# Optimization experiments

Hardware: AMD Instinct MI355X
Metric: run time of the kernel (lower is better)

The kernel has to match this reference:

```python
import jax, jax.numpy as jnp
import numpy as np

N = 200000      # active voxels
CIN = 96        # in_channels == out_channels (identity residual path)
CMID = 192      # max(in,out) * channel_multiplier
OFF = 27        # kernel_size**3 offsets
EPS = 1e-5      # BatchNorm eps


def setup_inputs() -> dict:
    key = jax.random.key(0)
    ks = jax.random.split(key, 6)
    x = jax.random.normal(ks[0], (N, CIN), jnp.float32)
    idx = jax.random.randint(ks[1], (OFF, N), 0, N, jnp.int32)
    mask = jax.random.randint(ks[2], (OFF, N), 0, 2, jnp.int32)
    W1 = jax.random.normal(ks[3], (OFF, CIN, CMID), jnp.float32) / np.float32(np.sqrt(OFF * CIN))
    W2 = jax.random.normal(ks[4], (OFF, CMID, CIN), jnp.float32) / np.float32(np.sqrt(OFF * CMID))
    g1 = jnp.ones((CMID,), jnp.float32)
    b1 = jnp.zeros((CMID,), jnp.float32)
    g2 = jnp.ones((CIN,), jnp.float32)
    b2 = jnp.zeros((CIN,), jnp.float32)
    return {"x": x, "idx": idx, "mask": mask, "W1": W1, "g1": g1, "b1": b1,
            "W2": W2, "g2": g2, "b2": b2}


def _sparse_conv(x, idx, mask, W):
    """Explicit-GEMM sparse conv: per-offset gather -> GEMM -> accumulate.
    x: [N, Cin], idx/mask: [OFF, N], W: [OFF, Cin, Cout] -> [N, Cout]."""
    n = x.shape[0]
    cout = W.shape[-1]

    def body(acc, off):
        i, m, w = off
        g = jnp.where(m[:, None] > 0, x[i], jnp.zeros((), x.dtype))  # gather [N, Cin]
        return acc + g @ w, None

    out, _ = jax.lax.scan(body, jnp.zeros((n, cout), x.dtype), (idx, mask, W))
    return out


def _bn(x, gamma, beta):
    # BatchNorm1d in training mode: batch statistics over the voxel dim.
    mu = jnp.mean(x, axis=0)
    var = jnp.var(x, axis=0)
    return gamma * (x - mu) * jax.lax.rsqrt(var + EPS) + beta


def reference(x, idx, mask, W1, g1, b1, W2, g2, b2):
    h = jax.nn.relu(_bn(_sparse_conv(x, idx, mask, W1), g1, b1))
    h = _bn(_sparse_conv(h, idx, mask, W2), g2, b2)
    return jax.nn.relu(h + x)  # identity residual (in_channels == out_channels)
```

## Files before the change

kernel.cpp:

```cpp
#include <hip/hip_runtime.h>
#include <hip/hip_bf16.h>

typedef unsigned short u16;
typedef __attribute__((ext_vector_type(8))) short short8;
typedef __attribute__((ext_vector_type(4))) float f32x4;
typedef __attribute__((ext_vector_type(8))) unsigned short ushort8v;

#define NVOX 200000
#define NOFF 27
#define NBLK 1563

__device__ __forceinline__ u16 f2bf(float f) {
    __hip_bfloat16 h = __float2bfloat16(f);
    return *reinterpret_cast<u16*>(&h);
}
__device__ __forceinline__ float bf2f(u16 u) {
    union { unsigned int i; float f; } v;
    v.i = ((unsigned int)u) << 16;
    return v.f;
}

#define GLOAD_LDS16(g, l)                                                     \
    __builtin_amdgcn_global_load_lds(                                         \
        (const __attribute__((address_space(1))) unsigned int*)(g),           \
        (__attribute__((address_space(3))) unsigned int*)(l), 16, 0, 0)

__global__ __launch_bounds__(256) void prep_kernel(
    const float* __restrict__ x, const float* __restrict__ W1,
    const float* __restrict__ W2, u16* __restrict__ xb,
    u16* __restrict__ w1t, u16* __restrict__ w2t, float* __restrict__ zbuf)
{
    const int XV = NVOX * 96 / 4;
    const int WC = 62208;
    int t = blockIdx.x * 256 + threadIdx.x;
    if (blockIdx.x == 0 && threadIdx.x < 64) zbuf[threadIdx.x] = 0.f;
    if (t < XV) {
        float4 v = *(const float4*)(x + (size_t)t * 4);
        ushort4 o;
        o.x = f2bf(v.x); o.y = f2bf(v.y); o.z = f2bf(v.z); o.w = f2bf(v.w);
        *(ushort4*)(xb + (size_t)t * 4) = o;
    } else if (t < XV + WC) {
        int j = t - XV;
        int lane = j & 63, rest = j >> 6;
        int nco = rest % 12, rest2 = rest / 12;
        int ks = rest2 % 3, off = rest2 / 3;
        int co = nco * 16 + (lane & 15);
        int kb = ks * 32 + (lane >> 4) * 8;
        const float* src = W1 + (size_t)off * 18432 + (size_t)kb * 192 + co;
        ushort8v ov;
#pragma unroll
        for (int jj = 0; jj < 8; ++jj) ov[jj] = f2bf(src[(size_t)jj * 192]);
        *(ushort8v*)(w1t + (size_t)j * 8) = ov;
    } else if (t < XV + 2 * WC) {
        int j = t - XV - WC;
        int lane = j & 63, rest = j >> 6;
        int nco = rest % 6, rest2 = rest / 6;
        int kk = rest2 % 6, off = rest2 / 6;
        int co = nco * 16 + (lane & 15);
        int kb = kk * 32 + (lane >> 4) * 8;
        const float* src = W2 + (size_t)off * 18432 + (size_t)kb * 96 + co;
        ushort8v ov;
#pragma unroll
        for (int jj = 0; jj < 8; ++jj) ov[jj] = f2bf(src[(size_t)jj * 96]);
        *(ushort8v*)(w2t + (size_t)j * 8) = ov;
    }
}

template<int COUT, int WN, int HFDIV>
__global__ __launch_bounds__(512, 4) void conv_mfma(
    const u16* __restrict__ xb, const int* __restrict__ idxp,
    const int* __restrict__ mskp, const u16* __restrict__ Wt,
    const float* __restrict__ zbuf, u16* __restrict__ hout,
    float* __restrict__ part)
{
    constexpr int CIN  = 96 * HFDIV;
    constexpr int WM   = 8 / WN;
    constexpr int FM   = 128 / (WM * 16);
    constexpr int FN   = COUT / (WN * 16);
    constexpr int NCO  = COUT / 16;
    constexpr int SG   = NOFF * HFDIV;
    constexpr int BUFU = 128 * 96;

    __shared__ u16 ldsA[2 * BUFU];
    __shared__ int lsrcL[NOFF * 128];

    const int tid  = threadIdx.x;
    const int row0 = blockIdx.x * 128;
    const int lane = tid & 63;
    const int wid  = tid >> 6;
    const int wm   = wid / WN;
    const int wn   = wid % WN;
    const int lr   = lane & 15;
    const int lk   = lane >> 4;

#pragma unroll
    for (int it = 0; it < 7; ++it) {
        int l = it * 512 + tid;
        if (l < NOFF * 128) {
            int o = l >> 7, r = row0 + (l & 127);
            int rr = r < NVOX ? r : NVOX - 1;
            int mv = mskp[(size_t)o * NVOX + rr];
            int iv = idxp[(size_t)o * NVOX + rr];
            lsrcL[l] = (r < NVOX && mv > 0) ? iv : -1;
        }
    }

    int aRow[3], aGcOff[3];
#pragma unroll
    for (int it = 0; it < 3; ++it) {
        int l = it * 512 + tid;
        int r = l / 12, c = l % 12;
        aRow[it] = r;
        aGcOff[it] = ((c + r) % 12) * 8;
    }
    int aBase[FM], d0m[FM];
#pragma unroll
    for (int m = 0; m < FM; ++m) {
        int r = wm * (FM * 16) + m * 16 + lr;
        aBase[m] = r * 96;
        d0m[m] = lk - (r % 12);
    }
    const u16* wtw = Wt + (size_t)(wn * FN) * 512 + (size_t)lane * 8;
    const int ldsWaveBase = (tid & ~63) * 8;

    f32x4 acc[FM][FN];
#pragma unroll
    for (int m = 0; m < FM; ++m)
#pragma unroll
        for (int n = 0; n < FN; ++n)
            acc[m][n] = (f32x4){0.f, 0.f, 0.f, 0.f};

    auto issueA = [&](int s, int bufSel) {
        int offIdx = (HFDIV == 1) ? s : (s >> 1);
        int hf     = (HFDIV == 1) ? 0 : (s & 1);
#pragma unroll
        for (int it = 0; it < 3; ++it) {
            int sv = lsrcL[offIdx * 128 + aRow[it]];
            const u16* g = (sv >= 0)
                ? (xb + (size_t)sv * CIN + hf * 96 + aGcOff[it])
                : ((const u16*)zbuf + aGcOff[it]);
            u16* d = ldsA + bufSel * BUFU + it * 512 * 8 + ldsWaveBase;
            GLOAD_LDS16(g, d);
        }
    };

    issueA(0, 0);
    short8 bfC[FN], bfN[FN];
#pragma unroll
    for (int n = 0; n < FN; ++n)
        bfC[n] = *(const short8*)(wtw + (size_t)n * 512);
    __syncthreads();

    int bufSel = 0;
#pragma unroll 1
    for (int s = 0; s < SG; ++s) {
        if (s + 1 < SG) issueA(s + 1, bufSel ^ 1);
        const u16* abuf = ldsA + bufSel * BUFU;
#pragma unroll
        for (int ks = 0; ks < 3; ++ks) {
            int nkidx = (ks < 2) ? (3 * s + ks + 1)
                                 : ((s + 1 < SG) ? 3 * (s + 1) : 3 * s + 2);
#pragma unroll
            for (int n = 0; n < FN; ++n)
                bfN[n] = *(const short8*)(wtw + ((size_t)nkidx * NCO + n) * 512);
            short8 af[FM];
#pragma unroll
            for (int m = 0; m < FM; ++m) {
                int c = ks * 4 + d0m[m];
                if (c < 0) c += 12;
                af[m] = *(const short8*)(abuf + aBase[m] + c * 8);
            }
#pragma unroll
            for (int n = 0; n < FN; ++n)
#pragma unroll
                for (int m = 0; m < FM; ++m)
                    acc[m][n] = __builtin_amdgcn_mfma_f32_16x16x32_bf16(
                        af[m], bfC[n], acc[m][n], 0, 0, 0);
#pragma unroll
            for (int n = 0; n < FN; ++n) bfC[n] = bfN[n];
        }
        __syncthreads();
        bufSel ^= 1;
    }

    float* smf = (float*)ldsA;
#pragma unroll
    for (int n = 0; n < FN; ++n) {
        float s1 = 0.f, s2 = 0.f;
#pragma unroll
        for (int m = 0; m < FM; ++m)
#pragma unroll
            for (int q = 0; q < 4; ++q) {
                float v = acc[m][n][q];
                s1 += v; s2 += v * v;
            }
        s1 += __shfl_xor(s1, 16); s1 += __shfl_xor(s1, 32);
        s2 += __shfl_xor(s2, 16); s2 += __shfl_xor(s2, 32);
        if (lane < 16) {
            int col = wn * (FN * 16) + n * 16 + lr;
            smf[(wm * COUT + col) * 2 + 0] = s1;
            smf[(wm * COUT + col) * 2 + 1] = s2;
        }
    }
    __syncthreads();
    if (tid < 2 * COUT) {
        int z = tid / COUT, cc = tid % COUT;
        float v = 0.f;
#pragma unroll
        for (int w = 0; w < WM; ++w) v += smf[(w * COUT + cc) * 2 + z];
        part[(size_t)blockIdx.x * (2 * COUT) + z * COUT + cc] = v;
    }

#pragma unroll
    for (int m = 0; m < FM; ++m) {
#pragma unroll
        for (int q = 0; q < 4; ++q) {
            int row = row0 + wm * (FM * 16) + m * 16 + lk * 4 + q;
            if (row < NVOX) {
#pragma unroll
                for (int n = 0; n < FN; ++n) {
                    int col = wn * (FN * 16) + n * 16 + lr;
                    hout[(size_t)row * COUT + col] = f2bf(acc[m][n][q]);
                }
            }
        }
    }
}

template<int COUT>
__global__ __launch_bounds__(256) void bn_statsB(
    const float* __restrict__ part, const float* __restrict__ g,
    const float* __restrict__ bv, float* __restrict__ ss)
{
    const int c = blockIdx.x;
    const int t = threadIdx.x;
    float s1 = 0.f, s2 = 0.f;
    for (int b = t; b < NBLK; b += 256) {
        s1 += part[(size_t)b * 2 * COUT + c];
        s2 += part[(size_t)b * 2 * COUT + COUT + c];
    }
#pragma unroll
    for (int d = 1; d < 64; d <<= 1) {
        s1 += __shfl_xor(s1, d);
        s2 += __shfl_xor(s2, d);
    }
    __shared__ float rs[8];
    int w = t >> 6;
    if ((t & 63) == 0) { rs[w] = s1; rs[4 + w] = s2; }
    __syncthreads();
    if (t == 0) {
        s1 = rs[0] + rs[1] + rs[2] + rs[3];
        s2 = rs[4] + rs[5] + rs[6] + rs[7];
        float mu  = s1 * (1.0f / NVOX);
        float var = s2 * (1.0f / NVOX) - mu * mu;
        float sc  = g[c] * rsqrtf(var + 1e-5f);
        ss[c] = sc;
        ss[COUT + c] = bv[c] - mu * sc;
    }
}

template<int COUT>
__global__ __launch_bounds__(256) void bn_apply_relu(
    u16* __restrict__ h, const float* __restrict__ ss)
{
    int t = blockIdx.x * 256 + threadIdx.x;
    int c0 = (t * 8) % COUT;
    ushort8v v = *(ushort8v*)(h + (size_t)t * 8);
#pragma unroll
    for (int j = 0; j < 8; ++j) {
        float f = bf2f(v[j]);
        f = fmaxf(f * ss[c0 + j] + ss[COUT + c0 + j], 0.f);
        v[j] = f2bf(f);
    }
    *(ushort8v*)(h + (size_t)t * 8) = v;
}

__global__ __launch_bounds__(256) void final_kernel(
    const u16* __restrict__ h2, const float* __restrict__ x,
    const float* __restrict__ ss, float* __restrict__ out)
{
    int t = blockIdx.x * 256 + threadIdx.x;
    int c0 = (t * 8) % 96;
    ushort8v v = *(const ushort8v*)(h2 + (size_t)t * 8);
    float4 x0 = *(const float4*)(x + (size_t)t * 8);
    float4 x1 = *(const float4*)(x + (size_t)t * 8 + 4);
    float xs[8] = {x0.x, x0.y, x0.z, x0.w, x1.x, x1.y, x1.z, x1.w};
    float o[8];
#pragma unroll
    for (int j = 0; j < 8; ++j) {
        float f = bf2f(v[j]) * ss[c0 + j] + ss[96 + c0 + j] + xs[j];
        o[j] = fmaxf(f, 0.f);
    }
    *(float4*)(out + (size_t)t * 8)     = (float4){o[0], o[1], o[2], o[3]};
    *(float4*)(out + (size_t)t * 8 + 4) = (float4){o[4], o[5], o[6], o[7]};
}

extern "C" void kernel_launch(void* const* d_in, const int* in_sizes, int n_in,
                              void* d_out, int out_size, void* d_ws, size_t ws_size,
                              hipStream_t stream)
{
    const float* x    = (const float*)d_in[0];
    const int*   idx  = (const int*)d_in[1];
    const int*   mask = (const int*)d_in[2];
    const float* W1   = (const float*)d_in[3];
    const float* g1   = (const float*)d_in[4];
    const float* b1   = (const float*)d_in[5];
    const float* W2   = (const float*)d_in[6];
    const float* g2   = (const float*)d_in[7];
    const float* b2   = (const float*)d_in[8];

    unsigned char* ws = (unsigned char*)d_ws;
    u16*  xb    = (u16*)ws;
    u16*  w1t   = (u16*)(ws + 38400000);
    u16*  w2t   = (u16*)(ws + 39395328);
    u16*  h2    = (u16*)(ws + 40390656);
    float* part = (float*)(ws + 78790656);
    float* ss1  = (float*)(ws + 81191424);
    float* ss2  = (float*)(ws + 81192960);
    float* zbuf = (float*)(ws + 81193728);

    u16* h = (u16*)d_out;

    prep_kernel<<<19236, 256, 0, stream>>>(x, W1, W2, xb, w1t, w2t, zbuf);

    conv_mfma<192, 4, 1><<<NBLK, 512, 0, stream>>>(xb, idx, mask, w1t, zbuf, h, part);
    bn_statsB<192><<<192, 256, 0, stream>>>(part, g1, b1, ss1);
    bn_apply_relu<192><<<18750, 256, 0, stream>>>(h, ss1);

    conv_mfma<96, 2, 2><<<NBLK, 512, 0, stream>>>(h, idx, mask, w2t, zbuf, h2, part);
    bn_statsB<96><<<96, 256, 0, stream>>>(part, g2, b2, ss2);
    final_kernel<<<9375, 256, 0, stream>>>(h2, x, ss2, (float*)d_out);
}
```

Baseline: 644.0 us.

## Precompute gather index table globally and shrink LDS to raise conv occupancy

```diff
diff --git a/kernel.cpp b/kernel.cpp
--- a/kernel.cpp
+++ b/kernel.cpp
@@ -7,6 +7,7 @@
 typedef __attribute__((ext_vector_type(8))) unsigned short ushort8v;
 
 #define NVOX 200000
+#define NVP  200064
 #define NOFF 27
 #define NBLK 1563
 
@@ -66,12 +67,26 @@
     }
 }
 
+__global__ __launch_bounds__(256) void lsrc_kernel(
+    const int* __restrict__ idxp, const int* __restrict__ mskp,
+    int* __restrict__ lsrcG)
+{
+    int r = blockIdx.x * 256 + threadIdx.x;
+    int o = blockIdx.y;
+    if (r < NVP) {
+        int v = -1;
+        if (r < NVOX) {
+            if (mskp[(size_t)o * NVOX + r] > 0) v = idxp[(size_t)o * NVOX + r];
+        }
+        lsrcG[(size_t)o * NVP + r] = v;
+    }
+}
+
 template<int COUT, int WN, int HFDIV>
-__global__ __launch_bounds__(512, 4) void conv_mfma(
-    const u16* __restrict__ xb, const int* __restrict__ idxp,
-    const int* __restrict__ mskp, const u16* __restrict__ Wt,
-    const float* __restrict__ zbuf, u16* __restrict__ hout,
-    float* __restrict__ part)
+__global__ __launch_bounds__(512, 6) void conv_mfma(
+    const u16* __restrict__ xb, const int* __restrict__ lsrcG,
+    const u16* __restrict__ Wt, const float* __restrict__ zbuf,
+    u16* __restrict__ hout, float* __restrict__ part)
 {
     constexpr int CIN  = 96 * HFDIV;
     constexpr int WM   = 8 / WN;
@@ -79,10 +94,9 @@
     constexpr int FN   = COUT / (WN * 16);
     constexpr int NCO  = COUT / 16;
     constexpr int SG   = NOFF * HFDIV;
-    constexpr int BUFU = 128 * 96;
+    constexpr int BUFU = 12 * 128 * 8;
 
     __shared__ u16 ldsA[2 * BUFU];
-    __shared__ int lsrcL[NOFF * 128];
 
     const int tid  = threadIdx.x;
     const int row0 = blockIdx.x * 128;
@@ -93,35 +107,17 @@
     const int lr   = lane & 15;
     const int lk   = lane >> 4;
 
-#pragma unroll
-    for (int it = 0; it < 7; ++it) {
-        int l = it * 512 + tid;
-        if (l < NOFF * 128) {
-            int o = l >> 7, r = row0 + (l & 127);
-            int rr = r < NVOX ? r : NVOX - 1;
-            int mv = mskp[(size_t)o * NVOX + rr];
-            int iv = idxp[(size_t)o * NVOX + rr];
-            lsrcL[l] = (r < NVOX && mv > 0) ? iv : -1;
-        }
-    }
-
-    int aRow[3], aGcOff[3];
-#pragma unroll
-    for (int it = 0; it < 3; ++it) {
-        int l = it * 512 + tid;
-        int r = l / 12, c = l % 12;
-        aRow[it] = r;
-        aGcOff[it] = ((c + r) % 12) * 8;
-    }
-    int aBase[FM], d0m[FM];
+    const int rStage = tid & 127;
+    const int c0 = tid >> 7;
+    const int ldsWaveBase = (tid & ~63) * 8;
+
+    int rdBase[FM];
 #pragma unroll
     for (int m = 0; m < FM; ++m) {
         int r = wm * (FM * 16) + m * 16 + lr;
-        aBase[m] = r * 96;
-        d0m[m] = lk - (r % 12);
+        rdBase[m] = r * 8 + lk * 1024;
     }
     const u16* wtw = Wt + (size_t)(wn * FN) * 512 + (size_t)lane * 8;
-    const int ldsWaveBase = (tid & ~63) * 8;
 
     f32x4 acc[FM][FN];
 #pragma unroll
@@ -133,22 +129,17 @@
     auto issueA = [&](int s, int bufSel) {
         int offIdx = (HFDIV == 1) ? s : (s >> 1);
         int hf     = (HFDIV == 1) ? 0 : (s & 1);
-#pragma unroll
-        for (int it = 0; it < 3; ++it) {
-            int sv = lsrcL[offIdx * 128 + aRow[it]];
-            const u16* g = (sv >= 0)
-                ? (xb + (size_t)sv * CIN + hf * 96 + aGcOff[it])
-                : ((const u16*)zbuf + aGcOff[it]);
-            u16* d = ldsA + bufSel * BUFU + it * 512 * 8 + ldsWaveBase;
-            GLOAD_LDS16(g, d);
-        }
+        int sv = lsrcG[(size_t)offIdx * NVP + row0 + rStage];
+        const u16* g = (sv >= 0)
+            ? (xb + (size_t)sv * CIN + hf * 96 + c0 * 8)
+            : ((const u16*)zbuf + c0 * 8);
+#pragma unroll
+        for (int it = 0; it < 3; ++it)
+            GLOAD_LDS16(g + it * 32,
+                        ldsA + bufSel * BUFU + it * 4096 + ldsWaveBase);
     };
 
     issueA(0, 0);
-    short8 bfC[FN], bfN[FN];
-#pragma unroll
-    for (int n = 0; n < FN; ++n)
-        bfC[n] = *(const short8*)(wtw + (size_t)n * 512);
     __syncthreads();
 
     int bufSel = 0;
@@ -158,26 +149,19 @@
         const u16* abuf = ldsA + bufSel * BUFU;
 #pragma unroll
         for (int ks = 0; ks < 3; ++ks) {
-            int nkidx = (ks < 2) ? (3 * s + ks + 1)
-                                 : ((s + 1 < SG) ? 3 * (s + 1) : 3 * s + 2);
+            int kidx = 3 * s + ks;
+            short8 bf_[FN];
 #pragma unroll
             for (int n = 0; n < FN; ++n)
-                bfN[n] = *(const short8*)(wtw + ((size_t)nkidx * NCO + n) * 512);
-            short8 af[FM];
+                bf_[n] = *(const short8*)(wtw + ((size_t)kidx * NCO + n) * 512);
 #pragma unroll
             for (int m = 0; m < FM; ++m) {
-                int c = ks * 4 + d0m[m];
-                if (c < 0) c += 12;
-                af[m] = *(const short8*)(abuf + aBase[m] + c * 8);
+                short8 af = *(const short8*)(abuf + rdBase[m] + ks * 4096);
+#pragma unroll
+                for (int n = 0; n < FN; ++n)
+                    acc[m][n] = __builtin_amdgcn_mfma_f32_16x16x32_bf16(
+                        af, bf_[n], acc[m][n], 0, 0, 0);
             }
-#pragma unroll
-            for (int n = 0; n < FN; ++n)
-#pragma unroll
-                for (int m = 0; m < FM; ++m)
-                    acc[m][n] = __builtin_amdgcn_mfma_f32_16x16x32_bf16(
-                        af[m], bfC[n], acc[m][n], 0, 0, 0);
-#pragma unroll
-            for (int n = 0; n < FN; ++n) bfC[n] = bfN[n];
         }
         __syncthreads();
         bufSel ^= 1;
@@ -318,16 +302,18 @@
     float* ss1  = (float*)(ws + 81191424);
     float* ss2  = (float*)(ws + 81192960);
     float* zbuf = (float*)(ws + 81193728);
+    int*  lsrcG = (int*)(ws + 81193984);
 
     u16* h = (u16*)d_out;
 
     prep_kernel<<<19236, 256, 0, stream>>>(x, W1, W2, xb, w1t, w2t, zbuf);
-
-    conv_mfma<192, 4, 1><<<NBLK, 512, 0, stream>>>(xb, idx, mask, w1t, zbuf, h, part);
+    lsrc_kernel<<<dim3(782, 27), 256, 0, stream>>>(idx, mask, lsrcG);
+
+    conv_mfma<192, 4, 1><<<NBLK, 512, 0, stream>>>(xb, lsrcG, w1t, zbuf, h, part);
     bn_statsB<192><<<192, 256, 0, stream>>>(part, g1, b1, ss1);
     bn_apply_relu<192><<<18750, 256, 0, stream>>>(h, ss1);
 
-    conv_mfma<96, 2, 2><<<NBLK, 512, 0, stream>>>(h, idx, mask, w2t, zbuf, h2, part);
+    conv_mfma<96, 2, 2><<<NBLK, 512, 0, stream>>>(h, lsrcG, w2t, zbuf, h2, part);
     bn_statsB<96><<<96, 256, 0, stream>>>(part, g2, b2, ss2);
     final_kernel<<<9375, 256, 0, stream>>>(h2, x, ss2, (float*)d_out);
 }
```

New measurement: 926.1 us. 43.8% more time.
